# Kernel tuning notes

Measured on AMD Instinct MI355X. Metric: run time of the kernel, lower is better.

The kernel has to match this reference:

```python
import jax, jax.numpy as jnp
import numpy as np

N = 50000       # nodes
E = 1_600_000   # edges (avg degree 32)
LAT, HID, OUT = 64, 128, 64


def _add_self_loops(edge_index, edge_attr, n):
    loop = jnp.arange(n, dtype=edge_index.dtype)
    src = jnp.concatenate([edge_index[0], loop])
    dst = jnp.concatenate([edge_index[1], loop])
    ew = jnp.concatenate([edge_attr, jnp.ones((n,), edge_attr.dtype)])
    return src, dst, ew


def _gcn_conv(x, W, b, src, dst, ew, n):
    # x: [N, Fin] -> [N, Fout]; GCN: D^{-1/2}(A+I)D^{-1/2} X W + b
    h = x @ W                                             # [N, Fout]
    deg = jax.ops.segment_sum(ew, dst, num_segments=n)    # weighted in-degree
    dinv = jnp.where(deg > 0, jax.lax.rsqrt(deg), 0.0)
    norm = dinv[src] * ew * dinv[dst]                     # [E+N]
    out = jax.ops.segment_sum(norm[:, None] * h[src], dst, num_segments=n)
    return out + b


def setup_inputs() -> dict:
    key = jax.random.key(0)
    k = jax.random.split(key, 8)
    z = jax.random.normal(k[0], (N, LAT), jnp.float32)
    edge_index = jax.random.randint(k[1], (2, E), 0, N, dtype=jnp.int32)
    edge_attr = jax.random.uniform(k[2], (E,), jnp.float32)
    W1 = jax.random.normal(k[3], (LAT, HID), jnp.float32) / np.sqrt(LAT)
    b1 = jnp.zeros((HID,), jnp.float32)
    W2 = jax.random.normal(k[4], (HID, OUT), jnp.float32) / np.sqrt(HID)
    b2 = jnp.zeros((OUT,), jnp.float32)
    return {"z": z, "edge_index": edge_index, "edge_attr": edge_attr,
            "W1": W1, "b1": b1, "W2": W2, "b2": b2}


def reference(z, edge_index, edge_attr, W1, b1, W2, b2):
    n = z.shape[0]
    src, dst, ew = _add_self_loops(edge_index, edge_attr, n)
    hidden = jax.nn.relu(_gcn_conv(z, W1, b1, src, dst, ew, n))
    return _gcn_conv(hidden, W2, b2, src, dst, ew, n)
```

## Files before the change

kernel.cpp:

```cpp
#include <hip/hip_runtime.h>


#define NPB 128
#define CH  8192

typedef __attribute__((ext_vector_type(8))) short short8v;
typedef __attribute__((ext_vector_type(4))) float f32x4;

__device__ __forceinline__ float4 ld4(const float* p) {
    return *reinterpret_cast<const float4*>(p);
}

__device__ __forceinline__ unsigned bfr(float f) {
    unsigned u = __float_as_uint(f);
    return (u + 0x7FFFu + ((u >> 16) & 1u)) >> 16;
}
__device__ __forceinline__ void bf2(unsigned v, float& lo, float& hi) {
    lo = __uint_as_float(v << 16);
    hi = __uint_as_float(v & 0xFFFF0000u);
}

__device__ __forceinline__ void scan_btot(const int* __restrict__ btot, int NBKT,
                                          int* bbs, int* wtot) {
    int tid = threadIdx.x;
    int v0 = (2 * tid     < NBKT) ? btot[2 * tid]     : 0;
    int v1 = (2 * tid + 1 < NBKT) ? btot[2 * tid + 1] : 0;
    int s = v0 + v1;
    int lane = tid & 63, wid = tid >> 6;
    int incl = s;
#pragma unroll
    for (int off = 1; off < 64; off <<= 1) {
        int u = __shfl_up(incl, off, 64);
        if (lane >= off) incl += u;
    }
    if (lane == 63) wtot[wid] = incl;
    __syncthreads();
    int woff = 0;
#pragma unroll
    for (int w = 0; w < 4; ++w) if (w < wid) woff += wtot[w];
    int ex = woff + incl - s;
    if (2 * tid     < NBKT) bbs[2 * tid]     = ex;
    if (2 * tid + 1 < NBKT) bbs[2 * tid + 1] = ex + v0;
    __syncthreads();
}

__global__ __launch_bounds__(256) void hist_kernel(const int* __restrict__ dst,
                                                   int* __restrict__ hist,
                                                   int E, int G1, int NBKT) {
    __shared__ int lh[512];
    for (int i = threadIdx.x; i < NBKT; i += 256) lh[i] = 0;
    __syncthreads();
    int g = blockIdx.x;
    int beg = g * CH, end = min(beg + CH, E);
    for (int j = beg + (int)threadIdx.x; j < end; j += 256)
        atomicAdd(&lh[dst[j] / NPB], 1);
    __syncthreads();
    for (int i = threadIdx.x; i < NBKT; i += 256) hist[(size_t)i * G1 + g] = lh[i];
}

__global__ __launch_bounds__(64) void bscan_kernel(int* __restrict__ hist,
                                                   int* __restrict__ btot, int G1) {
    int b = blockIdx.x;
    int* row = hist + (size_t)b * G1;
    int lane = threadIdx.x;
    int carry = 0;
    for (int g0 = 0; g0 < G1; g0 += 64) {
        int g = g0 + lane;
        int v = (g < G1) ? row[g] : 0;
        int incl = v;
#pragma unroll
        for (int off = 1; off < 64; off <<= 1) {
            int u = __shfl_up(incl, off, 64);
            if (lane >= off) incl += u;
        }
        if (g < G1) row[g] = carry + incl - v;
        carry += __shfl(incl, 63, 64);
    }
    if (lane == 0) btot[b] = carry;
}

__global__ __launch_bounds__(256) void scatter_kernel(const int* __restrict__ src,
                                                      const int* __restrict__ dst,
                                                      const float* __restrict__ ew,
                                                      const int* __restrict__ hist,
                                                      const int* __restrict__ btot,
                                                      int2* __restrict__ tmp,
                                                      int E, int G1, int NBKT) {
    __shared__ int bbs[512];
    __shared__ int wtot[4];
    __shared__ int cursor[512];
    scan_btot(btot, NBKT, bbs, wtot);
    int g = blockIdx.x;
    for (int i = threadIdx.x; i < NBKT; i += 256)
        cursor[i] = bbs[i] + hist[(size_t)i * G1 + g];
    __syncthreads();
    int beg = g * CH, end = min(beg + CH, E);
    for (int j = beg + (int)threadIdx.x; j < end; j += 256) {
        int d = dst[j];
        int b = d / NPB;
        int pos = atomicAdd(&cursor[b], 1);
        tmp[pos] = make_int2(((d & (NPB - 1)) << 24) | src[j], __float_as_int(ew[j]));
    }
}

__global__ __launch_bounds__(256) void finalize_kernel(const int2* __restrict__ tmp,
                                                       const int* __restrict__ btot,
                                                       const float* __restrict__ z,
                                                       int* __restrict__ rowptr,
                                                       float* __restrict__ dinv,
                                                       int2* __restrict__ csr,
                                                       uint2* __restrict__ zs,
                                                       int n, int E, int NBKT) {
    __shared__ int bbs[512];
    __shared__ int wsum_[4];
    __shared__ unsigned int hist[NPB];
    __shared__ float dvl[NPB];
    scan_btot(btot, NBKT, bbs, wsum_);
    int b = blockIdx.x;
    int base = bbs[b];
    int cnt  = btot[b];
    int tid  = threadIdx.x;
    if (tid < NPB) hist[tid] = 0;
    __syncthreads();
    for (int j = tid; j < cnt; j += 256) {
        int2 t = tmp[base + j];
        unsigned dlow = ((unsigned)t.x) >> 24;
        unsigned wfix = (unsigned)(__int_as_float(t.y) * 16384.0f);
        atomicAdd(&hist[dlow], (1u << 24) | wfix);
    }
    __syncthreads();
    int c = 0, incl = 0;
    unsigned pk = 0;
    if (tid < NPB) {
        pk = hist[tid];
        c = (int)(pk >> 24);
        incl = c;
#pragma unroll
        for (int off = 1; off < 64; off <<= 1) {
            int u = __shfl_up(incl, off, 64);
            if ((tid & 63) >= off) incl += u;
        }
        if ((tid & 63) == 63) wsum_[tid >> 6] = incl;
    }
    __syncthreads();
    if (tid < NPB) {
        int woff = (tid >= 64) ? wsum_[0] : 0;
        int excl = woff + incl - c;
        int node = b * NPB + tid;
        float dv = 0.f;
        if (node < n) {
            rowptr[node] = base + excl;
            float wdeg = (float)(pk & 0xFFFFFFu) * (1.0f / 16384.0f);
            dv = rsqrtf(wdeg + 1.0f);
            dinv[node] = dv;
        }
        dvl[tid]  = dv;
        hist[tid] = (unsigned)excl;
    }
    if (b == 0 && tid == 0) rowptr[n] = E;
    __syncthreads();
    for (int j = tid; j < cnt; j += 256) {
        int2 t = tmp[base + j];
        unsigned dlow = ((unsigned)t.x) >> 24;
        int srcv = t.x & 0xFFFFFF;
        int lr = (int)atomicAdd(&hist[dlow], 1u);
        csr[base + lr] = make_int2(srcv, t.y);
    }
    for (int t = tid; t < NPB * 16; t += 256) {
        int li = t >> 4;
        int node = b * NPB + li;
        if (node < n) {
            int k = t & 15;
            float dv = dvl[li];
            float4 f = ld4(z + (size_t)node * 64 + k * 4);
            zs[(size_t)node * 16 + k] =
                make_uint2(bfr(dv * f.x) | (bfr(dv * f.y) << 16),
                           bfr(dv * f.z) | (bfr(dv * f.w) << 16));
        }
    }
}

template<bool BIAS, bool OUTB>
__global__ __launch_bounds__(256) void gaggb_kernel(const int* __restrict__ rowptr,
                                                    const int2* __restrict__ csr,
                                                    const float* __restrict__ dinv,
                                                    const uint4* __restrict__ Hp4,
                                                    const float* __restrict__ b,
                                                    void* __restrict__ out, int n) {
    int row  = (blockIdx.x * 256 + threadIdx.x) >> 6;
    int lane = threadIdx.x & 63;
    if (row >= n) return;
    int eg = lane >> 3, fq = lane & 7;
    int beg = rowptr[row], end = rowptr[row + 1];
    float dv = dinv[row];

    float a0 = 0.f, a1 = 0.f, a2 = 0.f, a3 = 0.f;
    float a4 = 0.f, a5 = 0.f, a6 = 0.f, a7 = 0.f;
    float f0, f1, f2, f3, f4, f5, f6, f7;

#define ACCUM(V, W)                                            \
    bf2((V).x, f0, f1); bf2((V).y, f2, f3);                    \
    bf2((V).z, f4, f5); bf2((V).w, f6, f7);                    \
    a0 += (W) * f0; a1 += (W) * f1; a2 += (W) * f2; a3 += (W) * f3; \
    a4 += (W) * f4; a5 += (W) * f5; a6 += (W) * f6; a7 += (W) * f7;

    int j = beg;
    for (; j + 32 <= end; j += 32) {
        int2 m0 = csr[j + eg];
        int2 m1 = csr[j + eg + 8];
        int2 m2 = csr[j + eg + 16];
        int2 m3 = csr[j + eg + 24];
        uint4 v0 = Hp4[(size_t)(unsigned)(m0.x) * 8 + fq];
        uint4 v1 = Hp4[(size_t)(unsigned)(m1.x) * 8 + fq];
        uint4 v2 = Hp4[(size_t)(unsigned)(m2.x) * 8 + fq];
        uint4 v3 = Hp4[(size_t)(unsigned)(m3.x) * 8 + fq];
        float w0 = __int_as_float(m0.y), w1 = __int_as_float(m1.y);
        float w2 = __int_as_float(m2.y), w3 = __int_as_float(m3.y);
        ACCUM(v0, w0) ACCUM(v1, w1) ACCUM(v2, w2) ACCUM(v3, w3)
    }
    for (; j + 8 <= end; j += 8) {
        int2 m0 = csr[j + eg];
        float w0 = __int_as_float(m0.y);
        uint4 v0 = Hp4[(size_t)(unsigned)(m0.x) * 8 + fq];
        ACCUM(v0, w0)
    }
    if (j < end) {
        int idx = j + eg;
        if (idx < end) {
            int2 m0 = csr[idx];
            float w0 = __int_as_float(m0.y);
            uint4 v0 = Hp4[(size_t)(unsigned)(m0.x) * 8 + fq];
            ACCUM(v0, w0)
        }
    }
#undef ACCUM
#pragma unroll
    for (int off = 8; off < 64; off <<= 1) {
        a0 += __shfl_xor(a0, off, 64); a1 += __shfl_xor(a1, off, 64);
        a2 += __shfl_xor(a2, off, 64); a3 += __shfl_xor(a3, off, 64);
        a4 += __shfl_xor(a4, off, 64); a5 += __shfl_xor(a5, off, 64);
        a6 += __shfl_xor(a6, off, 64); a7 += __shfl_xor(a7, off, 64);
    }

    if (eg == 0) {
        uint4 sv = Hp4[(size_t)row * 8 + fq];
        float s0, s1, s2, s3, s4, s5, s6, s7;
        bf2(sv.x, s0, s1); bf2(sv.y, s2, s3);
        bf2(sv.z, s4, s5); bf2(sv.w, s6, s7);
        float o0 = dv * (a0 + s0), o1 = dv * (a1 + s1);
        float o2 = dv * (a2 + s2), o3 = dv * (a3 + s3);
        float o4 = dv * (a4 + s4), o5 = dv * (a5 + s5);
        float o6 = dv * (a6 + s6), o7 = dv * (a7 + s7);
        if (BIAS) {
            float4 b0 = ld4(b + fq * 8);
            float4 b1v = ld4(b + fq * 8 + 4);
            o0 += b0.x; o1 += b0.y; o2 += b0.z; o3 += b0.w;
            o4 += b1v.x; o5 += b1v.y; o6 += b1v.z; o7 += b1v.w;
        }
        if (OUTB) {
            uint4 pv = make_uint4(bfr(o0) | (bfr(o1) << 16),
                                  bfr(o2) | (bfr(o3) << 16),
                                  bfr(o4) | (bfr(o5) << 16),
                                  bfr(o6) | (bfr(o7) << 16));
            reinterpret_cast<uint4*>(out)[(size_t)row * 8 + fq] = pv;
        } else {
            float4* op = reinterpret_cast<float4*>((float*)out + (size_t)row * 64 + fq * 8);
            op[0] = make_float4(o0, o1, o2, o3);
            op[1] = make_float4(o4, o5, o6, o7);
        }
    }
}

__global__ __launch_bounds__(256) void densemfma_kernel(
        const unsigned short* __restrict__ t1b,
        const float* __restrict__ W1,
        const float* __restrict__ b1,
        const float* __restrict__ W2,
        const float* __restrict__ dinv,
        unsigned short* __restrict__ hs,
        int n) {
    __shared__ __align__(16) unsigned short W1s[128][68];
    __shared__ __align__(16) unsigned short W2s[64][132];
    __shared__ float b1s[128];
    __shared__ __align__(16) unsigned short hT[4][16][136];
    for (int i = threadIdx.x; i < 128 * 64; i += 256) {
        int c = i >> 6, k = i & 63;
        W1s[c][k] = (unsigned short)bfr(W1[k * 128 + c]);
    }
    for (int i = threadIdx.x; i < 64 * 128; i += 256) {
        int c = i >> 7, k = i & 127;
        W2s[c][k] = (unsigned short)bfr(W2[k * 64 + c]);
    }
    if (threadIdx.x < 128) b1s[threadIdx.x] = b1[threadIdx.x];
    __syncthreads();

    int wv = threadIdx.x >> 6;
    int l  = threadIdx.x & 63;
    int m  = l & 15, g = l >> 4;
    int ngrp = (n + 63) >> 6;
    for (int grp = blockIdx.x; grp < ngrp; grp += gridDim.x) {
        int R = grp * 64 + wv * 16;
        short8v a0 = {0,0,0,0,0,0,0,0}, a1 = {0,0,0,0,0,0,0,0};
        int rowA = R + m;
        if (rowA < n) {
            a0 = *reinterpret_cast<const short8v*>(t1b + (size_t)rowA * 64 + 8 * g);
            a1 = *reinterpret_cast<const short8v*>(t1b + (size_t)rowA * 64 + 32 + 8 * g);
        }
#pragma unroll
        for (int ct = 0; ct < 8; ++ct) {
            short8v wb0 = *reinterpret_cast<const short8v*>(&W1s[ct * 16 + m][8 * g]);
            short8v wb1 = *reinterpret_cast<const short8v*>(&W1s[ct * 16 + m][32 + 8 * g]);
            f32x4 c = {0.f, 0.f, 0.f, 0.f};
            c = __builtin_amdgcn_mfma_f32_16x16x32_bf16(a0, wb0, c, 0, 0, 0);
            c = __builtin_amdgcn_mfma_f32_16x16x32_bf16(a1, wb1, c, 0, 0, 0);
            float bb = b1s[ct * 16 + m];
#pragma unroll
            for (int r = 0; r < 4; ++r) {
                float v = fmaxf(c[r] + bb, 0.f);
                hT[wv][4 * g + r][ct * 16 + m] = (unsigned short)bfr(v);
            }
        }
        f32x4 acc2[4];
#pragma unroll
        for (int ct = 0; ct < 4; ++ct) acc2[ct] = (f32x4){0.f, 0.f, 0.f, 0.f};
#pragma unroll
        for (int kk = 0; kk < 4; ++kk) {
            short8v ha = *reinterpret_cast<const short8v*>(&hT[wv][m][kk * 32 + 8 * g]);
#pragma unroll
            for (int ct = 0; ct < 4; ++ct) {
                short8v wb = *reinterpret_cast<const short8v*>(
                    &W2s[ct * 16 + m][kk * 32 + 8 * g]);
                acc2[ct] = __builtin_amdgcn_mfma_f32_16x16x32_bf16(ha, wb, acc2[ct], 0, 0, 0);
            }
        }
#pragma unroll
        for (int r = 0; r < 4; ++r) {
            int grow = R + 4 * g + r;
            float dv = (grow < n) ? dinv[grow] : 0.f;
#pragma unroll
            for (int ct = 0; ct < 4; ++ct)
                hT[wv][4 * g + r][ct * 16 + m] = (unsigned short)bfr(acc2[ct][r] * dv);
        }
        int growO = R + m;
        if (growO < n) {
            uint4 u0 = *reinterpret_cast<const uint4*>(&hT[wv][m][g * 16]);
            uint4 u1 = *reinterpret_cast<const uint4*>(&hT[wv][m][g * 16 + 8]);
            *reinterpret_cast<uint4*>(hs + (size_t)growO * 64 + g * 16) = u0;
            *reinterpret_cast<uint4*>(hs + (size_t)growO * 64 + g * 16 + 8) = u1;
        }
    }
}

extern "C" void kernel_launch(void* const* d_in, const int* in_sizes, int n_in,
                              void* d_out, int out_size, void* d_ws, size_t ws_size,
                              hipStream_t stream) {
    const float* z  = (const float*)d_in[0];
    const int*   ei = (const int*)d_in[1];
    const float* ea = (const float*)d_in[2];
    const float* W1 = (const float*)d_in[3];
    const float* b1 = (const float*)d_in[4];
    const float* W2 = (const float*)d_in[5];
    const float* b2 = (const float*)d_in[6];
    float* out = (float*)d_out;

    const int n = in_sizes[0] / 64;
    const int E = in_sizes[2];
    const int* src = ei;
    const int* dst = ei + E;
    const int NBKT = (n + NPB - 1) / NPB;
    const int G1   = (E + CH - 1) / CH;

    float* ws = (float*)d_ws;
    size_t p = 0;
    auto alloc = [&](size_t elems) { size_t o = p; p += (elems + 63) & ~63ull; return o; };
    float* dinv   = ws + alloc(n);
    int*   rowptr = (int*)(ws + alloc((size_t)n + 1));
    int*   btot   = (int*)(ws + alloc(NBKT));
    int2*  csr    = (int2*)(ws + alloc((size_t)E * 2));
    unsigned short* t1b = (unsigned short*)(ws + alloc((size_t)n * 32));
    uint2* zs     = (uint2*)(ws + alloc((size_t)n * 32));
    float* X      = ws + alloc((size_t)E * 2 + (size_t)NBKT * G1 + 64);
    int2*  tmp    = (int2*)X;
    int*   hist   = (int*)(X + (size_t)E * 2);
    (void)ws_size;

    hist_kernel<<<G1, 256, 0, stream>>>(dst, hist, E, G1, NBKT);
    bscan_kernel<<<NBKT, 64, 0, stream>>>(hist, btot, G1);
    scatter_kernel<<<G1, 256, 0, stream>>>(src, dst, ea, hist, btot, tmp, E, G1, NBKT);
    finalize_kernel<<<NBKT, 256, 0, stream>>>(tmp, btot, z, rowptr, dinv,
                                              csr, zs, n, E, NBKT);

    const int gblocks = (n + 3) / 4;
    gaggb_kernel<false, true><<<gblocks, 256, 0, stream>>>(rowptr, csr, dinv,
                                                           (const uint4*)zs,
                                                           nullptr, t1b, n);
    densemfma_kernel<<<256, 256, 0, stream>>>(t1b, W1, b1, W2, dinv,
                                              (unsigned short*)zs, n);
    gaggb_kernel<true, false><<<gblocks, 256, 0, stream>>>(rowptr, csr, dinv,
                                                           (const uint4*)zs,
                                                           b2, out, n);
}
```

Before: 146.9 us.

## Pack CSR edges into 32-bit src/bf16-weight words and halve node bucket size

Each CSR entry is now a single 32-bit word: the source index in the low 16 bits and the edge weight rounded to bf16 in the high 16 bits. This halves the edge-stream bytes read by both aggregation passes. The node bucket size drops from 128 to 64, so the per-bucket degree scan in finalize fits in one wavefront and needs no cross-wave sync; shared arrays and the bucket scan are widened to handle twice as many buckets. The costs are that edge weights lose precision and source indices must stay below 65536, which holds for this graph size but would break larger graphs.

```diff
diff --git a/kernel.cpp b/kernel.cpp
--- a/kernel.cpp
+++ b/kernel.cpp
@@ -1,7 +1,7 @@
 #include <hip/hip_runtime.h>
 
 
-#define NPB 128
+#define NPB 64
 #define CH  8192
 
 typedef __attribute__((ext_vector_type(8))) short short8v;
@@ -23,9 +23,14 @@
 __device__ __forceinline__ void scan_btot(const int* __restrict__ btot, int NBKT,
                                           int* bbs, int* wtot) {
     int tid = threadIdx.x;
-    int v0 = (2 * tid     < NBKT) ? btot[2 * tid]     : 0;
-    int v1 = (2 * tid + 1 < NBKT) ? btot[2 * tid + 1] : 0;
-    int s = v0 + v1;
+    int v[4];
+    int s = 0;
+#pragma unroll
+    for (int q = 0; q < 4; ++q) {
+        int i = 4 * tid + q;
+        v[q] = (i < NBKT) ? btot[i] : 0;
+        s += v[q];
+    }
     int lane = tid & 63, wid = tid >> 6;
     int incl = s;
 #pragma unroll
@@ -39,15 +44,19 @@
 #pragma unroll
     for (int w = 0; w < 4; ++w) if (w < wid) woff += wtot[w];
     int ex = woff + incl - s;
-    if (2 * tid     < NBKT) bbs[2 * tid]     = ex;
-    if (2 * tid + 1 < NBKT) bbs[2 * tid + 1] = ex + v0;
+#pragma unroll
+    for (int q = 0; q < 4; ++q) {
+        int i = 4 * tid + q;
+        if (i < NBKT) bbs[i] = ex;
+        ex += v[q];
+    }
     __syncthreads();
 }
 
 __global__ __launch_bounds__(256) void hist_kernel(const int* __restrict__ dst,
                                                    int* __restrict__ hist,
                                                    int E, int G1, int NBKT) {
-    __shared__ int lh[512];
+    __shared__ int lh[1024];
     for (int i = threadIdx.x; i < NBKT; i += 256) lh[i] = 0;
     __syncthreads();
     int g = blockIdx.x;
@@ -86,9 +95,9 @@
                                                       const int* __restrict__ btot,
                                                       int2* __restrict__ tmp,
                                                       int E, int G1, int NBKT) {
-    __shared__ int bbs[512];
+    __shared__ int bbs[1024];
     __shared__ int wtot[4];
-    __shared__ int cursor[512];
+    __shared__ int cursor[1024];
     scan_btot(btot, NBKT, bbs, wtot);
     int g = blockIdx.x;
     for (int i = threadIdx.x; i < NBKT; i += 256)
@@ -108,10 +117,10 @@
                                                        const float* __restrict__ z,
                                                        int* __restrict__ rowptr,
                                                        float* __restrict__ dinv,
-                                                       int2* __restrict__ csr,
+                                                       unsigned* __restrict__ csr,
                                                        uint2* __restrict__ zs,
                                                        int n, int E, int NBKT) {
-    __shared__ int bbs[512];
+    __shared__ int bbs[1024];
     __shared__ int wsum_[4];
     __shared__ unsigned int hist[NPB];
     __shared__ float dvl[NPB];
@@ -129,23 +138,16 @@
         atomicAdd(&hist[dlow], (1u << 24) | wfix);
     }
     __syncthreads();
-    int c = 0, incl = 0;
-    unsigned pk = 0;
     if (tid < NPB) {
-        pk = hist[tid];
-        c = (int)(pk >> 24);
-        incl = c;
+        unsigned pk = hist[tid];
+        int c = (int)(pk >> 24);
+        int incl = c;
 #pragma unroll
         for (int off = 1; off < 64; off <<= 1) {
             int u = __shfl_up(incl, off, 64);
-            if ((tid & 63) >= off) incl += u;
-        }
-        if ((tid & 63) == 63) wsum_[tid >> 6] = incl;
-    }
-    __syncthreads();
-    if (tid < NPB) {
-        int woff = (tid >= 64) ? wsum_[0] : 0;
-        int excl = woff + incl - c;
+            if (tid >= off) incl += u;
+        }
+        int excl = incl - c;
         int node = b * NPB + tid;
         float dv = 0.f;
         if (node < n) {
@@ -162,9 +164,9 @@
     for (int j = tid; j < cnt; j += 256) {
         int2 t = tmp[base + j];
         unsigned dlow = ((unsigned)t.x) >> 24;
-        int srcv = t.x & 0xFFFFFF;
+        unsigned srcv = (unsigned)(t.x & 0xFFFFFF);
         int lr = (int)atomicAdd(&hist[dlow], 1u);
-        csr[base + lr] = make_int2(srcv, t.y);
+        csr[base + lr] = srcv | (bfr(__int_as_float(t.y)) << 16);
     }
     for (int t = tid; t < NPB * 16; t += 256) {
         int li = t >> 4;
@@ -182,7 +184,7 @@
 
 template<bool BIAS, bool OUTB>
 __global__ __launch_bounds__(256) void gaggb_kernel(const int* __restrict__ rowptr,
-                                                    const int2* __restrict__ csr,
+                                                    const unsigned* __restrict__ csr,
                                                     const float* __restrict__ dinv,
                                                     const uint4* __restrict__ Hp4,
                                                     const float* __restrict__ b,
@@ -206,30 +208,32 @@
 
     int j = beg;
     for (; j + 32 <= end; j += 32) {
-        int2 m0 = csr[j + eg];
-        int2 m1 = csr[j + eg + 8];
-        int2 m2 = csr[j + eg + 16];
-        int2 m3 = csr[j + eg + 24];
-        uint4 v0 = Hp4[(size_t)(unsigned)(m0.x) * 8 + fq];
-        uint4 v1 = Hp4[(size_t)(unsigned)(m1.x) * 8 + fq];
-        uint4 v2 = Hp4[(size_t)(unsigned)(m2.x) * 8 + fq];
-        uint4 v3 = Hp4[(size_t)(unsigned)(m3.x) * 8 + fq];
-        float w0 = __int_as_float(m0.y), w1 = __int_as_float(m1.y);
-        float w2 = __int_as_float(m2.y), w3 = __int_as_float(m3.y);
+        unsigned m0 = csr[j + eg];
+        unsigned m1 = csr[j + eg + 8];
+        unsigned m2 = csr[j + eg + 16];
+        unsigned m3 = csr[j + eg + 24];
+        uint4 v0 = Hp4[(size_t)(m0 & 0xFFFFu) * 8 + fq];
+        uint4 v1 = Hp4[(size_t)(m1 & 0xFFFFu) * 8 + fq];
+        uint4 v2 = Hp4[(size_t)(m2 & 0xFFFFu) * 8 + fq];
+        uint4 v3 = Hp4[(size_t)(m3 & 0xFFFFu) * 8 + fq];
+        float w0 = __uint_as_float(m0 & 0xFFFF0000u);
+        float w1 = __uint_as_float(m1 & 0xFFFF0000u);
+        float w2 = __uint_as_float(m2 & 0xFFFF0000u);
+        float w3 = __uint_as_float(m3 & 0xFFFF0000u);
         ACCUM(v0, w0) ACCUM(v1, w1) ACCUM(v2, w2) ACCUM(v3, w3)
     }
     for (; j + 8 <= end; j += 8) {
-        int2 m0 = csr[j + eg];
-        float w0 = __int_as_float(m0.y);
-        uint4 v0 = Hp4[(size_t)(unsigned)(m0.x) * 8 + fq];
+        unsigned m0 = csr[j + eg];
+        float w0 = __uint_as_float(m0 & 0xFFFF0000u);
+        uint4 v0 = Hp4[(size_t)(m0 & 0xFFFFu) * 8 + fq];
         ACCUM(v0, w0)
     }
     if (j < end) {
         int idx = j + eg;
         if (idx < end) {
-            int2 m0 = csr[idx];
-            float w0 = __int_as_float(m0.y);
-            uint4 v0 = Hp4[(size_t)(unsigned)(m0.x) * 8 + fq];
+            unsigned m0 = csr[idx];
+            float w0 = __uint_as_float(m0 & 0xFFFF0000u);
+            uint4 v0 = Hp4[(size_t)(m0 & 0xFFFFu) * 8 + fq];
             ACCUM(v0, w0)
         }
     }
@@ -373,15 +377,15 @@
     float* ws = (float*)d_ws;
     size_t p = 0;
     auto alloc = [&](size_t elems) { size_t o = p; p += (elems + 63) & ~63ull; return o; };
-    float* dinv   = ws + alloc(n);
-    int*   rowptr = (int*)(ws + alloc((size_t)n + 1));
-    int*   btot   = (int*)(ws + alloc(NBKT));
-    int2*  csr    = (int2*)(ws + alloc((size_t)E * 2));
+    float*    dinv   = ws + alloc(n);
+    int*      rowptr = (int*)(ws + alloc((size_t)n + 1));
+    int*      btot   = (int*)(ws + alloc(NBKT));
+    unsigned* csr    = (unsigned*)(ws + alloc(E));
     unsigned short* t1b = (unsigned short*)(ws + alloc((size_t)n * 32));
-    uint2* zs     = (uint2*)(ws + alloc((size_t)n * 32));
-    float* X      = ws + alloc((size_t)E * 2 + (size_t)NBKT * G1 + 64);
-    int2*  tmp    = (int2*)X;
-    int*   hist   = (int*)(X + (size_t)E * 2);
+    uint2*    zs     = (uint2*)(ws + alloc((size_t)n * 32));
+    float*    X      = ws + alloc((size_t)E * 2 + (size_t)NBKT * G1 + 64);
+    int2*     tmp    = (int2*)X;
+    int*      hist   = (int*)(X + (size_t)E * 2);
     (void)ws_size;
 
     hist_kernel<<<G1, 256, 0, stream>>>(dst, hist, E, G1, NBKT);
```

Measured after the change: 143.7 us. -2.2%, faster.
